# Optimization experiments

Measured on AMD Instinct MI355X. Metric: run time of the kernel, lower is better.

Reference implementation:

```python
import jax, jax.numpy as jnp
import numpy as np

B, N, FEAT, BB, LD = 512, 50, 300, 300, 2048
D1 = BB + FEAT        # 600 = s_with_bb dim
D2 = 2 * D1           # 1200 = combined dim


def _fc(x, w, b):
    # ReLUWithWeightNormFC: weight-norm is a reparametrization of a plain
    # linear, so math-equivalently ReLU(x @ W^T + b).
    return jax.nn.relu(x @ w.T + b)


def setup_inputs() -> dict:
    key = jax.random.key(0)
    ks = jax.random.split(key, 32)

    def p(k, shape):
        return jax.random.normal(k, shape, dtype=jnp.float32) * 0.02

    inp = {
        "l": jax.random.normal(ks[0], (B, LD), dtype=jnp.float32),
        "s": jax.random.normal(ks[1], (B, N, FEAT), dtype=jnp.float32),
        "ps": jax.random.uniform(ks[2], (B, N, 4), dtype=jnp.float32),
        "mask_s": jax.random.randint(ks[3], (B,), 0, 50, dtype=jnp.int32),
        "bb_w": p(ks[4], (BB, 10)),       "bb_b": p(ks[5], (BB,)),
        "fa1_w": p(ks[6], (D1, D1)),      "fa1_b": p(ks[7], (D1,)),
        "fa2_w": p(ks[8], (D1, D1)),      "fa2_b": p(ks[9], (D1,)),
        "fa3_w": p(ks[10], (D2, D2)),     "fa3_b": p(ks[11], (D2,)),
        "fa4_w": p(ks[12], (D2, D2)),     "fa4_b": p(ks[13], (D2,)),
        "fa5_w": p(ks[14], (D2, D2)),     "fa5_b": p(ks[15], (D2,)),
        "lp1_w": p(ks[16], (D2, LD)),     "lp1_b": p(ks[17], (D2,)),
        "lp2_w": p(ks[18], (D2, LD)),     "lp2_b": p(ks[19], (D2,)),
        "out_w": p(ks[20], (FEAT, D2)),   "out_b": p(ks[21], (FEAT,)),
    }
    return inp


def reference(l, s, ps, mask_s,
              bb_w, bb_b, fa1_w, fa1_b, fa2_w, fa2_b, fa3_w, fa3_b,
              fa4_w, fa4_b, fa5_w, fa5_b, lp1_w, lp1_b, lp2_w, lp2_b,
              out_w, out_b):
    # ---- bb_process ----
    size = ps[..., 2:] - ps[..., :2]                       # [B,N,2]
    centre = ps[..., :2] + 0.5 * size                      # [B,N,2]
    area = (size[..., 0] * size[..., 1])[..., None]        # [B,N,1]
    shape = (size[..., 0] / (size[..., 1] + 1e-14))[..., None]
    bb_in = jnp.concatenate([ps, size, centre, area, shape], axis=-1)  # [B,N,10]
    bb = _fc(bb_in, bb_w, bb_b)                            # [B,N,BB]

    s_bb = jnp.concatenate([s, bb], axis=-1)               # [B,N,D1]

    # ---- masked adjacency bias (order of assignments preserved) ----
    i = jnp.arange(N)
    mx = jnp.maximum(i[None, :], i[:, None])               # [N,N]
    m1 = mx[None, :, :] < mask_s[:, None, None]            # [B,N,N]
    m2 = i[None, :, None] >= mask_s[:, None, None]         # row index >= mask_s
    inf_tmp = jnp.where(m1 | m2, 0.0, -jnp.inf)
    inf_tmp = jnp.where(jnp.eye(N, dtype=bool)[None], -jnp.inf, inf_tmp)
    inf_tmp = inf_tmp.at[:, 0, 0].set(
        jnp.where(mask_s == 1, 0.0, inf_tmp[:, 0, 0]))

    # l projections are identical across the 50 nodes -> compute once, broadcast
    lp1 = _fc(l, lp1_w, lp1_b)[:, None, :]                 # [B,1,D2]
    lp2 = _fc(l, lp2_w, lp2_b)[:, None, :]                 # [B,1,D2]

    # ---- one GNN iteration (it=1) ----
    combined = jnp.concatenate(
        [s_bb, _fc(s_bb, fa1_w, fa1_b) * _fc(s_bb, fa2_w, fa2_b)], axis=-1)  # [B,N,D2]
    l_masked_source = _fc(combined, fa3_w, fa3_b) * lp1    # [B,N,D2]
    adj = jnp.einsum('bnd,bmd->bnm', _fc(combined, fa4_w, fa4_b),
                     l_masked_source)                      # [B,N,N]
    adj = jax.nn.softmax(adj + inf_tmp, axis=2)
    prepared = _fc(combined, fa5_w, fa5_b) * lp2           # [B,N,D2]
    messages = _fc(jnp.einsum('bnm,bmd->bnd', adj, prepared), out_w, out_b)
    s_out = jnp.concatenate([s, messages], axis=-1)        # [B,N,2*FEAT]

    output_mask = (i[None, :] < mask_s[:, None])[:, :, None]  # [B,N,1]
    return s_out * output_mask.astype(s_out.dtype), adj
```

## Files before the change

### kernel.cpp

```cpp
#include <hip/hip_runtime.h>
#include <stdint.h>

typedef unsigned short u16;
typedef unsigned int u32;
typedef __attribute__((ext_vector_type(8))) __bf16 bf16x8;
typedef __attribute__((ext_vector_type(4))) float f32x4;

#define DEVINL static __device__ __forceinline__

DEVINL u16 f2bf(float x) {
  u32 u = __float_as_uint(x);
  return (u16)((u + (((u >> 16) & 1u) + 0x7fffu)) >> 16);
}
DEVINL float bf2f(u16 h) { return __uint_as_float(((u32)h) << 16); }

DEVINL void async16(const void* g, void* l) {
  void* g2 = const_cast<void*>(g);
  __builtin_amdgcn_global_load_lds((__attribute__((address_space(1))) void*)g2,
                                   (__attribute__((address_space(3))) void*)l,
                                   16, 0, 0);
}

DEVINL void swz_xy(int& bx, int& by) {
  const int gx = (int)gridDim.x;
// ... 82 lines not shown
  const int p1 = ((c1 & 3) ^ ((c1 >> 3) & 3)) * 8;
  const long ao0 = (long)(c0 >> 2) * lda + p0;
  const long ao1 = (long)(c1 >> 2) * lda + p1;
  const long bo0 = (long)(c0 >> 2) * ldw + p0;
  const long bo1 = (long)(c1 >> 2) * ldw + p1;

  int aoffs[4], boffs[4];
#pragma unroll
  for (int k = 0; k < 4; ++k) {
    const int ra = wr + mrow + 16 * k;
    const int rb = wc + mrow + 16 * k;
    aoffs[k] = ra * 32 + ((q ^ ((ra >> 1) & 3)) << 3);
    boffs[k] = rb * 32 + ((q ^ ((rb >> 1) & 3)) << 3);
  }

  auto issueF = [&](int ph) {
    const long ta = (long)(ph >> 1) * 32;
    const u16* sa = (ph & 1) ? Alp : Ahp;
    const u16* sb = (ph & 1) ? Blp : Bhp;
    u16* d = S + (ph & 3) * 8192;
    async16(sa + ta + ao0, d + c0 * 8);
    async16(sa + ta + ao1, d + c1 * 8);
    async16(sb + ta + bo0, d + 4096 + c0 * 8);
    async16(sb + ta + bo1, d + 4096 + c1 * 8);
  };

  const int total = 2 * ksteps;
  issueF(0); issueF(1); if (total > 2) issueF(2);
  bf16x8 ah[4], bh[4];
  for (int i = 0; i < ksteps; ++i) {
    {
      const int rem = total - 1 - 2 * i;
      if (rem >= 2)      asm volatile("s_waitcnt vmcnt(8)" ::: "memory");
      else               asm volatile("s_waitcnt vmcnt(4)" ::: "memory");
      __builtin_amdgcn_sched_barrier(0);
      __builtin_amdgcn_s_barrier();
      __builtin_amdgcn_sched_barrier(0);
      if (2 * i + 3 < total) issueF(2 * i + 3);
      const u16* hb = S + ((2 * i) & 3) * 8192;
#pragma unroll
      for (int k = 0; k < 4; ++k) {
        ah[k] = *(const bf16x8*)(hb + aoffs[k]);
        bh[k] = *(const bf16x8*)(hb + 4096 + boffs[k]);
      }
#pragma unroll
      for (int mi = 0; mi < 4; ++mi)
#pragma unroll
        for (int nj = 0; nj < 4; ++nj)
          acc[mi][nj] = __builtin_amdgcn_mfma_f32_16x16x32_bf16(
              ah[mi], bh[nj], acc[mi][nj], 0, 0, 0);
    }
    {
      const int rem = total - 2 - 2 * i;
      if (rem >= 2)      asm volatile("s_waitcnt vmcnt(8)" ::: "memory");
      else if (rem == 1) asm volatile("s_waitcnt vmcnt(4)" ::: "memory");
      else               asm volatile("s_waitcnt vmcnt(0)" ::: "memory");
      __builtin_amdgcn_sched_barrier(0);
      __builtin_amdgcn_s_barrier();
      __builtin_amdgcn_sched_barrier(0);
      if (2 * i + 4 < total) issueF(2 * i + 4);
      const u16* hb = S + ((2 * i + 1) & 3) * 8192;
      bf16x8 al[4], bl[4];
#pragma unroll
      for (int k = 0; k < 4; ++k) {
        al[k] = *(const bf16x8*)(hb + aoffs[k]);
        bl[k] = *(const bf16x8*)(hb + 4096 + boffs[k]);
      }
#pragma unroll
      for (int mi = 0; mi < 4; ++mi)
#pragma unroll
        for (int nj = 0; nj < 4; ++nj)
          acc[mi][nj] = __builtin_amdgcn_mfma_f32_16x16x32_bf16(
              al[mi], bh[nj], acc[mi][nj], 0, 0, 0);
#pragma unroll
      for (int mi = 0; mi < 4; ++mi)
#pragma unroll
        for (int nj = 0; nj < 4; ++nj)
          acc[mi][nj] = __builtin_amdgcn_mfma_f32_16x16x32_bf16(
              ah[mi], bl[nj], acc[mi][nj], 0, 0, 0);
    }
  }
}

DEVINL void gemm_core1(const u16* Ab, const u16* Bb, int lda, int ldw,
                       int ksteps, u16* As, u16* Bs, f32x4 (&acc)[4][4]) {
  const int tid = threadIdx.x;
  const int lane = tid & 63;
  const int wv = tid >> 6;
  const int wr = (wv >> 1) * 64;
  const int wc = (wv & 1) * 64;
  const int mrow = lane & 15;
  const int q = lane >> 4;

  const int c0 = tid, c1 = tid + 256;
  const int p0 = ((c0 & 3) ^ ((c0 >> 3) & 3)) * 8;
  const int p1 = ((c1 & 3) ^ ((c1 >> 3) & 3)) * 8;
  const long ao0 = (long)(c0 >> 2) * lda + p0;
  const long ao1 = (long)(c1 >> 2) * lda + p1;
  const long bo0 = (long)(c0 >> 2) * ldw + p0;
  const long bo1 = (long)(c1 >> 2) * ldw + p1;

  int aoffs[4], boffs[4];
#pragma unroll
  for (int k = 0; k < 4; ++k) {
    const int ra = wr + mrow + 16 * k;
    const int rb = wc + mrow + 16 * k;
    aoffs[k] = ra * 32 + ((q ^ ((ra >> 1) & 3)) << 3);
    boffs[k] = rb * 32 + ((q ^ ((rb >> 1) & 3)) << 3);
  }

  auto issue = [&](int sl, int t) {
    const long ta = (long)t * 32;
    u16* dA = As + sl * 4096;
    u16* dB = Bs + sl * 4096;
    async16(Ab + ta + ao0, dA + c0 * 8);
    async16(Ab + ta + ao1, dA + c1 * 8);
    async16(Bb + ta + bo0, dB + c0 * 8);
    async16(Bb + ta + bo1, dB + c1 * 8);
  };

  const int npro = ksteps < 3 ? ksteps : 3;
  for (int j = 0; j < npro; ++j) issue(j, j);
  int cs = 0, is = 3;
  for (int i = 0; i < ksteps; ++i) {
    const int rem = ksteps - 1 - i;
    if (rem >= 2)      asm volatile("s_waitcnt vmcnt(8)" ::: "memory");
    else if (rem == 1) asm volatile("s_waitcnt vmcnt(4)" ::: "memory");
    else               asm volatile("s_waitcnt vmcnt(0)" ::: "memory");
    __builtin_amdgcn_sched_barrier(0);
    __builtin_amdgcn_s_barrier();
    __builtin_amdgcn_sched_barrier(0);
    if (i + 3 < ksteps) { issue(is, i + 3); is = (is + 1) & 3; }
    const u16* Sa = As + cs * 4096;
    const u16* Sb = Bs + cs * 4096;
    cs = (cs + 1) & 3;
    bf16x8 af[4], bv[4];
#pragma unroll
    for (int k = 0; k < 4; ++k) af[k] = *(const bf16x8*)(Sa + aoffs[k]);
#pragma unroll
    for (int k = 0; k < 4; ++k) bv[k] = *(const bf16x8*)(Sb + boffs[k]);
#pragma unroll
    for (int mi = 0; mi < 4; ++mi)
#pragma unroll
      for (int nj = 0; nj < 4; ++nj)
        acc[mi][nj] = __builtin_amdgcn_mfma_f32_16x16x32_bf16(
            af[mi], bv[nj], acc[mi][nj], 0, 0, 0);
  }
}

DEVINL void gemm_core2(const u16* const Aph[3], const u16* const B1ph[3],
                       const u16* const B2ph[3], int lda, int ldw, int ksteps,
                       u16* As, u16* B1s, u16* B2s, f32x4 (&a1)[4][4],
                       f32x4 (&a2)[4][4]) {
  const int tid = threadIdx.x;
  const int lane = tid & 63;
  const int wv = tid >> 6;
  const int wr = (wv >> 1) * 64;
  const int wc = (wv & 1) * 64;
  const int mrow = lane & 15;
  const int q = lane >> 4;

  const int c0 = tid, c1 = tid + 256;
  const int p0 = ((c0 & 3) ^ ((c0 >> 3) & 3)) * 8;
  const int p1 = ((c1 & 3) ^ ((c1 >> 3) & 3)) * 8;
  const long ao0 = (long)(c0 >> 2) * lda + p0;
  const long ao1 = (long)(c1 >> 2) * lda + p1;
  const long bo0 = (long)(c0 >> 2) * ldw + p0;
  const long bo1 = (long)(c1 >> 2) * ldw + p1;

  int aoffs[4], boffs[4];
#pragma unroll
  for (int k = 0; k < 4; ++k) {
    const int ra = wr + mrow + 16 * k;
    const int rb = wc + mrow + 16 * k;
    aoffs[k] = ra * 32 + ((q ^ ((ra >> 1) & 3)) << 3);
    boffs[k] = rb * 32 + ((q ^ ((rb >> 1) & 3)) << 3);
  }

  const u16* Aa1 = Aph[1]; const u16* Ba1 = B1ph[1]; const u16* Ca1 = B2ph[1];
  const u16* Aa2 = Aph[2]; const u16* Ba2 = B1ph[2]; const u16* Ca2 = B2ph[2];
  const u16* An = Aph[0];  const u16* Bn = B1ph[0];  const u16* Cn = B2ph[0];
  int tn = 0, pn = 0;
  const int total = 3 * ksteps;

  auto issue = [&](int sl) {
    const u16* ga = An + (long)tn * 32;
    const u16* g1 = Bn + (long)tn * 32;
    const u16* g2 = Cn + (long)tn * 32;
    u16* dA = As + sl * 4096;
    u16* d1 = B1s + sl * 4096;
    u16* d2 = B2s + sl * 4096;
    async16(ga + ao0, dA + c0 * 8);
    async16(ga + ao1, dA + c1 * 8);
    async16(g1 + bo0, d1 + c0 * 8);
    async16(g1 + bo1, d1 + c1 * 8);
    async16(g2 + bo0, d2 + c0 * 8);
    async16(g2 + bo1, d2 + c1 * 8);
    if (++tn == ksteps) {
      tn = 0; ++pn;
      if (pn == 1) { An = Aa1; Bn = Ba1; Cn = Ca1; }
      else if (pn == 2) { An = Aa2; Bn = Ba2; Cn = Ca2; }
    }
  };

  issue(0);
  issue(1);
  int slot = 0;
  for (int i = 0; i < total; ++i) {
    if (i + 1 < total) asm volatile("s_waitcnt vmcnt(6)" ::: "memory");
    else               asm volatile("s_waitcnt vmcnt(0)" ::: "memory");
    __builtin_amdgcn_sched_barrier(0);
    __builtin_amdgcn_s_barrier();
    __builtin_amdgcn_sched_barrier(0);
    if (i + 2 < total) {
      int s2 = slot + 2; if (s2 >= 3) s2 -= 3;
      issue(s2);
    }
    const u16* Sa = As + slot * 4096;
    const u16* S1 = B1s + slot * 4096;
    const u16* S2 = B2s + slot * 4096;
    bf16x8 af[4], b1v[4], b2v[4];
#pragma unroll
    for (int k = 0; k < 4; ++k) af[k] = *(const bf16x8*)(Sa + aoffs[k]);
#pragma unroll
    for (int k = 0; k < 4; ++k) b1v[k] = *(const bf16x8*)(S1 + boffs[k]);
#pragma unroll
    for (int k = 0; k < 4; ++k) b2v[k] = *(const bf16x8*)(S2 + boffs[k]);
#pragma unroll
    for (int mi = 0; mi < 4; ++mi)
#pragma unroll
      for (int nj = 0; nj < 4; ++nj)
        a1[mi][nj] = __builtin_amdgcn_mfma_f32_16x16x32_bf16(
            af[mi], b1v[nj], a1[mi][nj], 0, 0, 0);
#pragma unroll
    for (int mi = 0; mi < 4; ++mi)
#pragma unroll
      for (int nj = 0; nj < 4; ++nj)
        a2[mi][nj] = __builtin_amdgcn_mfma_f32_16x16x32_bf16(
            af[mi], b2v[nj], a2[mi][nj], 0, 0, 0);
    if (++slot == 3) slot = 0;
  }
}

#define GEMM_EPI_IDX                                                    \
  const int lane = threadIdx.x & 63, wv = threadIdx.x >> 6;             \
  const int wr = (wv >> 1) * 64, wc = (wv & 1) * 64;                    \
  const int mcol = lane & 15, q = lane >> 4;                            \
  const int gm0 = by * 128, gn0 = bx * 128;

__global__ __launch_bounds__(256) void k_gemm_fa12(const u16* Ah, const u16* Al,
    const u16* W1h, const u16* W1l, const u16* W2h, const u16* W2l,
    const float* bias, u16* Chi, u16* Clo) {
  __shared__ __align__(16) u16 As[12288], B1s[12288], B2s[12288];
  int bx, by; swz_xy(bx, by);
  const size_t arow = (size_t)by * 128 * 1280;
  const size_t wrow = (size_t)bx * 128 * 640;
  const u16* Aph[3]  = {Ah + arow, Al + arow, Ah + arow};
  const u16* B1ph[3] = {W1h + wrow, W1h + wrow, W1l + wrow};
  const u16* B2ph[3] = {W2h + wrow, W2h + wrow, W2l + wrow};
  f32x4 a1[4][4] = {}, a2[4][4] = {};
  gemm_core2(Aph, B1ph, B2ph, 1280, 640, 20, As, B1s, B2s, a1, a2);
  GEMM_EPI_IDX
#pragma unroll
  for (int mi = 0; mi < 4; ++mi)
#pragma unroll
    for (int r = 0; r < 4; ++r) {
      int grow = gm0 + wr + mi * 16 + q * 4 + r;
#pragma unroll
      for (int ni = 0; ni < 4; ++ni) {
        int gcol = gn0 + wc + ni * 16 + mcol;
        float v1 = fmaxf(a1[mi][ni][r] + bias[gcol], 0.f);
        float v2 = fmaxf(a2[mi][ni][r] + bias[640 + gcol], 0.f);
        float y = v1 * v2;
        u16 h = f2bf(y);
        Chi[(size_t)grow * 1280 + 640 + gcol] = h;
        Clo[(size_t)grow * 1280 + 640 + gcol] = f2bf(y - bf2f(h));
      }
    }
}

__global__ __launch_bounds__(256) void k_gemm_lp(const u16* Ah, const u16* Al,
    const u16* Wh, const u16* Wl, const float* bias, float* outp) {
  __shared__ __align__(16) u16 S[32768];
  int bx, by; swz_xy(bx, by);
  const size_t arow = (size_t)by * 128 * 2048;
  const size_t wrow = (size_t)bx * 128 * 2048;
  f32x4 acc[4][4] = {};
  gemm_fused3(Ah + arow, Al + arow, Wh + wrow, Wl + wrow, 2048, 2048, 64, S,
              acc);
  GEMM_EPI_IDX
#pragma unroll
  for (int mi = 0; mi < 4; ++mi)
#pragma unroll
    for (int r = 0; r < 4; ++r) {
      int grow = gm0 + wr + mi * 16 + q * 4 + r;
#pragma unroll
      for (int ni = 0; ni < 4; ++ni) {
        int gcol = gn0 + wc + ni * 16 + mcol;
        outp[(size_t)grow * 2560 + gcol] = fmaxf(acc[mi][ni][r] + bias[gcol], 0.f);
      }
    }
}

__global__ __launch_bounds__(512, 2) void k_gemm_fa34(const u16* Ah,
    const u16* Al, const u16* Wh, const u16* Wl, const float* b34,
    const float* lp_o, u16* fa3h, u16* fa3l, u16* fa4h, u16* fa4l, int r0) {
  __shared__ __align__(16) u16 S[2][4][8192];
  int bx, by; swz_xy(bx, by);
  const int tid = threadIdx.x;
  const int lane = tid & 63, wv = tid >> 6;
  const int wm = wv >> 2, wn = wv & 3;
  const int mrow = lane & 15, q = lane >> 4;

  const size_t arow = (size_t)by * 256 * 1280;
  const size_t wrow = (size_t)bx * 256 * 1280;
  const u16* mats[4] = {Ah + arow, Al + arow, Wh + wrow, Wl + wrow};

  long soff[2];
#pragma unroll
  for (int j = 0; j < 2; ++j) {
    const int c = j * 512 + tid;
    soff[j] = (long)(c >> 2) * 1280 + ((c & 3) ^ ((c >> 3) & 3)) * 8;
  }
  int aoffs[8], boffs[4];
#pragma unroll
  for (int k = 0; k < 8; ++k) {
    const int r = wm * 128 + k * 16 + mrow;
    aoffs[k] = r * 32 + ((q ^ ((r >> 1) & 3)) << 3);
  }
#pragma unroll
  for (int k = 0; k < 4; ++k) {
    const int r = wn * 64 + k * 16 + mrow;
    boffs[k] = r * 32 + ((q ^ ((r >> 1) & 3)) << 3);
  }

  f32x4 acc[8][4] = {};
  const int ks = 40;

#pragma unroll
  for (int m = 0; m < 4; ++m) {
    async16(mats[m] + soff[0], &S[0][m][tid * 8]);
    async16(mats[m] + soff[1], &S[0][m][(512 + tid) * 8]);
  }
  asm volatile("s_waitcnt vmcnt(0)" ::: "memory");
  __builtin_amdgcn_sched_barrier(0);
  __builtin_amdgcn_s_barrier();

  for (int t = 0; t < ks; ++t) {
    const int cur = t & 1;
    const long ta = (long)(t + 1) * 32;
    const bool more = (t + 1 < ks);
    bf16x8 bh[4], bl[4];
#pragma unroll
    for (int p = 0; p < 8; ++p) {
      if (p == 0) {
#pragma unroll
        for (int k = 0; k < 4; ++k) {
          bh[k] = *(const bf16x8*)(&S[cur][2][0] + boffs[k]);
          bl[k] = *(const bf16x8*)(&S[cur][3][0] + boffs[k]);
        }
      }
      bf16x8 ah = *(const bf16x8*)(&S[cur][0][0] + aoffs[p]);
      bf16x8 al = *(const bf16x8*)(&S[cur][1][0] + aoffs[p]);
      if (p < 4 && more) {
        async16(mats[p] + ta + soff[0], &S[cur ^ 1][p][tid * 8]);
        async16(mats[p] + ta + soff[1], &S[cur ^ 1][p][(512 + tid) * 8]);
      }
      __builtin_amdgcn_s_barrier();
      asm volatile("s_waitcnt lgkmcnt(0)" ::: "memory");
      __builtin_amdgcn_sched_barrier(0);
      __builtin_amdgcn_s_setprio(1);
#pragma unroll
      for (int j = 0; j < 4; ++j)
        acc[p][j] = __builtin_amdgcn_mfma_f32_16x16x32_bf16(ah, bh[j],
                                                            acc[p][j], 0, 0, 0);
#pragma unroll
      for (int j = 0; j < 4; ++j)
        acc[p][j] = __builtin_amdgcn_mfma_f32_16x16x32_bf16(al, bh[j],
                                                            acc[p][j], 0, 0, 0);
#pragma unroll
      for (int j = 0; j < 4; ++j)
        acc[p][j] = __builtin_amdgcn_mfma_f32_16x16x32_bf16(ah, bl[j],
                                                            acc[p][j], 0, 0, 0);
      __builtin_amdgcn_s_setprio(0);
      __builtin_amdgcn_s_barrier();
    }
    if (more) {
      asm volatile("s_waitcnt vmcnt(0)" ::: "memory");
      __builtin_amdgcn_sched_barrier(0);
      __builtin_amdgcn_s_barrier();
    }
  }

  const int gm0 = by * 256, gn0 = bx * 256;
  const int seg = (gn0 >= 1280);
  u16* dsth = seg ? fa4h : fa3h;
  u16* dstl = seg ? fa4l : fa3l;
#pragma unroll
  for (int p = 0; p < 8; ++p)
#pragma unroll
    for (int r = 0; r < 4; ++r) {
      const int grow = gm0 + wm * 128 + p * 16 + q * 4 + r;
      const int b = (r0 + grow) / 50;
      const float* lpb = lp_o + (size_t)b * 2560;
#pragma unroll
      for (int j = 0; j < 4; ++j) {
        const int gcol = gn0 + wn * 64 + j * 16 + mrow;
        const int c = gcol - seg * 1280;
        float v = fmaxf(acc[p][j][r] + b34[gcol], 0.f);
        if (!seg) v *= lpb[c];
        if (c < 1216) {
          u16 h = f2bf(v);
          dsth[(size_t)grow * 1216 + c] = h;
          dstl[(size_t)grow * 1216 + c] = f2bf(v - bf2f(h));
        }
      }
    }
}

__global__ __launch_bounds__(256) void k_gemm_fa5(const u16* Ah,
    const u16* W5h, const float* b5, const float* lp_o, u16* fa5o, int r0) {
  __shared__ __align__(16) u16 S[32768];
  int bx, by; swz_xy(bx, by);
  const size_t arow = (size_t)by * 128 * 1280;
  const size_t wrow = (size_t)bx * 128 * 1280;
  f32x4 acc[4][4] = {};
  gemm_core1(Ah + arow, W5h + wrow, 1280, 1280, 40, S, S + 16384, acc);
  GEMM_EPI_IDX
#pragma unroll
  for (int mi = 0; mi < 4; ++mi)
#pragma unroll
    for (int r = 0; r < 4; ++r) {
      int grow = gm0 + wr + mi * 16 + q * 4 + r;
      int b = (r0 + grow) / 50;
      const float* lpb = lp_o + (size_t)b * 2560 + 1280;
#pragma unroll
      for (int ni = 0; ni < 4; ++ni) {
        int gcol = gn0 + wc + ni * 16 + mcol;
        float v = fmaxf(acc[mi][ni][r] + b5[gcol], 0.f) * lpb[gcol];
        if (gcol < 1216) fa5o[(size_t)grow * 1216 + gcol] = f2bf(v);
      }
    }
}

__global__ __launch_bounds__(256) void k_gemm_out(const u16* A, const u16* Wh,
    const float* bias, const int* mask_s, float* outp, int r0) {
  __shared__ __align__(16) u16 S[32768];
  int bx, by; swz_xy(bx, by);
  const size_t arow = (size_t)by * 128 * 1216;
  const size_t wrow = (size_t)bx * 128 * 1216;
  f32x4 acc[4][4] = {};
  gemm_core1(A + arow, Wh + wrow, 1216, 1216, 38, S, S + 16384, acc);
  GEMM_EPI_IDX
#pragma unroll
  for (int mi = 0; mi < 4; ++mi)
#pragma unroll
    for (int r = 0; r < 4; ++r) {
      int grow = r0 + gm0 + wr + mi * 16 + q * 4 + r;
      int b = grow / 50;
      int n = grow - b * 50;
      float keep = (n < mask_s[b]) ? 1.f : 0.f;
#pragma unroll
      for (int ni = 0; ni < 4; ++ni) {
        int gcol = gn0 + wc + ni * 16 + mcol;
        float v = fmaxf(acc[mi][ni][r] + bias[gcol], 0.f) * keep;
        if (gcol < 300) outp[(size_t)grow * 600 + 300 + gcol] = v;
      }
    }
}

__global__ __launch_bounds__(256) void k_attn(const u16* fa3h, const u16* fa3l,
    const u16* fa4h, const u16* fa4l, const u16* fa5o, const int* mask_s,
    float* adj_out, u16* msg, int b0) {
  __shared__ __align__(16) u16 stg[32768];
  __shared__ float Ssc[64 * 64];
  const int bl = blockIdx.x;
  const int bg = b0 + bl;
  const int tid = threadIdx.x, lane = tid & 63, wv = tid >> 6;
  const int mrow = lane & 15, q = lane >> 4;
  const size_t base = (size_t)bl * 50 * 1216;

  {
    const int srow = tid >> 2;
    const int srcRow = srow < 50 ? srow : 49;
    const size_t gsoff = base + (size_t)srcRow * 1216 +
                         (size_t)(((tid & 3) ^ ((tid >> 3) & 3)) * 8);
    auto issueP1 = [&](int sl, int s) {
      const int p = (s >= 76) ? 2 : (s >= 38 ? 1 : 0);
      const int t = s - p * 38;
      const u16* Ap = (p == 1) ? fa4l : fa4h;
      const u16* Bp = (p == 2) ? fa3l : fa3h;
      u16* d = stg + sl * 4096;
      async16(Ap + gsoff + (size_t)t * 32, d + tid * 8);
      async16(Bp + gsoff + (size_t)t * 32, d + 2048 + tid * 8);
    };
    const int ra = wv * 16 + mrow;
    const int aoff = ra * 32 + ((q ^ ((ra >> 1) & 3)) << 3);
    int boff[4];
#pragma unroll
    for (int ni = 0; ni < 4; ++ni) {
      const int rb = ni * 16 + mrow;
      boff[ni] = rb * 32 + ((q ^ ((rb >> 1) & 3)) << 3);
    }
    for (int j = 0; j < 7; ++j) issueP1(j, j);
    f32x4 acc[4] = {};
    int cs = 0, is = 7;
    for (int i = 0; i < 114; ++i) {
      const int rem = 113 - i;
      if (rem >= 6)      asm volatile("s_waitcnt vmcnt(12)" ::: "memory");
      else if (rem == 5) asm volatile("s_waitcnt vmcnt(10)" ::: "memory");
      else if (rem == 4) asm volatile("s_waitcnt vmcnt(8)" ::: "memory");
      else if (rem == 3) asm volatile("s_waitcnt vmcnt(6)" ::: "memory");
      else if (rem == 2) asm volatile("s_waitcnt vmcnt(4)" ::: "memory");
      else if (rem == 1) asm volatile("s_waitcnt vmcnt(2)" ::: "memory");
      else               asm volatile("s_waitcnt vmcnt(0)" ::: "memory");
      __builtin_amdgcn_sched_barrier(0);
      __builtin_amdgcn_s_barrier();
      __builtin_amdgcn_sched_barrier(0);
      if (i + 7 < 114) { issueP1(is, i + 7); if (++is == 8) is = 0; }
      const u16* d = stg + cs * 4096;
      if (++cs == 8) cs = 0;
      bf16x8 af = *(const bf16x8*)(d + aoff);
#pragma unroll
      for (int ni = 0; ni < 4; ++ni) {
        bf16x8 bv = *(const bf16x8*)(d + 2048 + boff[ni]);
        acc[ni] =
            __builtin_amdgcn_mfma_f32_16x16x32_bf16(af, bv, acc[ni], 0, 0, 0);
      }
    }
#pragma unroll
    for (int ni = 0; ni < 4; ++ni)
#pragma unroll
      for (int r = 0; r < 4; ++r)
        Ssc[(wv * 16 + q * 4 + r) * 64 + ni * 16 + mrow] = acc[ni][r];
  }
  __syncthreads();

  const int c0 = tid, c1 = tid + 256;
  const int m0 = c0 >> 3, d0 = (c0 & 7) * 8;
  const int m1 = c1 >> 3, d1 = (c1 & 7) * 8;
  const size_t g0 = base + (size_t)(m0 < 50 ? m0 : 49) * 1216 + d0;
  const size_t g1 = base + (size_t)(m1 < 50 ? m1 : 49) * 1216 + d1;
  auto issueP3 = [&](int sl, int s) {
    u16* d = stg + sl * 4096;
    async16(fa5o + g0 + (size_t)s * 64, d + c0 * 8);
    async16(fa5o + g1 + (size_t)s * 64, d + c1 * 8);
  };
  for (int j = 0; j < 7; ++j) issueP3(j, j);

  {
    const int mk = mask_s[bg];
    for (int n = wv; n < 50; n += 4) {
      int mm = lane;
      float v = -__builtin_inff();
      if (mm < 50) {
        int mx2 = n > mm ? n : mm;
        bool valid = (mx2 < mk) || (n >= mk);
        if (mm == n) valid = false;
        if (n == 0 && mm == 0 && mk == 1) valid = true;
        if (valid) v = Ssc[n * 64 + mm];
      }
      float mx = v;
      for (int o = 32; o > 0; o >>= 1) mx = fmaxf(mx, __shfl_down(mx, o));
      mx = __shfl(mx, 0);
      float e = __expf(v - mx);
      float sm = e;
      for (int o = 32; o > 0; o >>= 1) sm += __shfl_down(sm, o);
      sm = __shfl(sm, 0);
      float pv = e / sm;
      if (mm < 50) {
        adj_out[((size_t)bg * 50 + n) * 50 + mm] = pv;
        Ssc[n * 64 + mm] = pv;
      } else {
        Ssc[n * 64 + mm] = 0.f;
      }
    }
  }
  __syncthreads();

  {
    int cs = 0, is = 7;
    for (int dt = 0; dt < 19; ++dt) {
      const int rem = 18 - dt;
      if (rem >= 6)      asm volatile("s_waitcnt vmcnt(12)" ::: "memory");
      else if (rem == 5) asm volatile("s_waitcnt vmcnt(10)" ::: "memory");
      else if (rem == 4) asm volatile("s_waitcnt vmcnt(8)" ::: "memory");
      else if (rem == 3) asm volatile("s_waitcnt vmcnt(6)" ::: "memory");
      else if (rem == 2) asm volatile("s_waitcnt vmcnt(4)" ::: "memory");
      else if (rem == 1) asm volatile("s_waitcnt vmcnt(2)" ::: "memory");
      else               asm volatile("s_waitcnt vmcnt(0)" ::: "memory");
      __builtin_amdgcn_sched_barrier(0);
      __builtin_amdgcn_s_barrier();
      __builtin_amdgcn_sched_barrier(0);
      if (dt + 7 < 19) { issueP3(is, dt + 7); if (++is == 8) is = 0; }
      const u16* d = stg + cs * 4096;
      if (++cs == 8) cs = 0;
      f32x4 a3[4] = {};
#pragma unroll
      for (int ks = 0; ks < 2; ++ks) {
        bf16x8 af;
#pragma unroll
        for (int j = 0; j < 8; ++j)
          af[j] = (__bf16)Ssc[(wv * 16 + mrow) * 64 + ks * 32 + q * 8 + j];
#pragma unroll
        for (int ni = 0; ni < 4; ++ni) {
          bf16x8 bv;
#pragma unroll
          for (int j = 0; j < 8; ++j)
            bv[j] = *(const __bf16*)(d + (ks * 32 + q * 8 + j) * 64 + ni * 16 + mrow);
          a3[ni] = __builtin_amdgcn_mfma_f32_16x16x32_bf16(af, bv, a3[ni], 0, 0, 0);
        }
      }
#pragma unroll
      for (int ni = 0; ni < 4; ++ni)
#pragma unroll
        for (int r = 0; r < 4; ++r) {
          int n = wv * 16 + q * 4 + r;
          if (n < 50)
            msg[((size_t)bl * 50 + n) * 1216 + dt * 64 + ni * 16 + mrow] =
                f2bf(a3[ni][r]);
        }
    }
  }
}

extern "C" void kernel_launch(void* const* d_in, const int* in_sizes, int n_in,
                              void* d_out_, int out_size, void* d_ws,
                              size_t ws_size, hipStream_t stream) {
  (void)in_sizes; (void)n_in; (void)out_size;
  const float* l_in = (const float*)d_in[0];
  const float* s_in = (const float*)d_in[1];
  const float* ps   = (const float*)d_in[2];
  const int*   msk  = (const int*)d_in[3];
  const float* bbw  = (const float*)d_in[4];
  const float* bbb  = (const float*)d_in[5];
  const float* fa1w = (const float*)d_in[6];
  const float* fa1b = (const float*)d_in[7];
  const float* fa2w = (const float*)d_in[8];
  const float* fa2b = (const float*)d_in[9];
  const float* fa3w = (const float*)d_in[10];
  const float* fa3b = (const float*)d_in[11];
  const float* fa4w = (const float*)d_in[12];
  const float* fa4b = (const float*)d_in[13];
  const float* fa5w = (const float*)d_in[14];
  const float* fa5b = (const float*)d_in[15];
  const float* lp1w = (const float*)d_in[16];
  const float* lp1b = (const float*)d_in[17];
  const float* lp2w = (const float*)d_in[18];
  const float* lp2b = (const float*)d_in[19];
  const float* outw = (const float*)d_in[20];
  const float* outb = (const float*)d_in[21];
  float* outp = (float*)d_out_;

  char* wsb = (char*)d_ws;
  size_t off = 0;
  auto alloc = [&](size_t bytes) -> char* {
    char* p = wsb + off;
    off = (off + bytes + 255) & ~(size_t)255;
    return p;
  };
  u16*   l_hi   = (u16*)alloc(512ull * 2048 * 2);
  u16*   l_lo   = (u16*)alloc(512ull * 2048 * 2);
  u16*   Wout   = (u16*)alloc(384ull * 1216 * 2);
  float* b_fa12 = (float*)alloc(1280 * 4);
  float* b_fa34 = (float*)alloc(2560 * 4);
  float* b_fa5  = (float*)alloc(1280 * 4);
  float* b_lp   = (float*)alloc(2560 * 4);
  float* b_out  = (float*)alloc(384 * 4);
  float* lp_o   = (float*)alloc(512ull * 2560 * 4);
  u16*   slab   = (u16*)alloc(10485760ull * 2);
  u16* Wlph   = slab;
  u16* Wlpl   = slab + 5242880;
  u16* Wfa1h  = slab;
  u16* Wfa1l  = slab + 409600;
  u16* Wfa2h  = slab + 819200;
  u16* Wfa2l  = slab + 1228800;
  u16* Wfa34h = slab + 1638400;
  u16* Wfa34l = slab + 4915200;
  u16* Wfa5h  = slab + 8192000;

  size_t ws_eff = ws_size ? ws_size : (size_t)512 * 1024 * 1024;
  long RN = 6400;
  const long opts[3] = {25600, 12800, 6400};
  for (int i = 0; i < 3; ++i) {
    size_t need = off + (size_t)17280 * opts[i] + 8 * 256;
    if (need <= ws_eff) { RN = opts[i]; break; }
  }
  u16*  Chi  = (u16*)alloc((size_t)RN * 1280 * 2);
  u16*  Clo  = (u16*)alloc((size_t)RN * 1280 * 2);
  u16*  fa5o = (u16*)alloc((size_t)RN * 1216 * 2);
  u16*  fa3h = (u16*)alloc((size_t)RN * 1216 * 2);
  u16*  fa3l = (u16*)alloc((size_t)RN * 1216 * 2);
  u16*  fa4h = (u16*)alloc((size_t)RN * 1216 * 2);
  u16*  fa4l = (u16*)alloc((size_t)RN * 1216 * 2);
  u16*  msg  = Chi;
  float* adj_o = outp + 15360000;

  dim3 T(256);
  k_pack_bias<<<dim3(3), T, 0, stream>>>(fa1b, 600, b_fa12, 640);
  k_pack_bias<<<dim3(3), T, 0, stream>>>(fa2b, 600, b_fa12 + 640, 640);
  k_pack_bias<<<dim3(5), T, 0, stream>>>(fa3b, 1200, b_fa34, 1280);
  k_pack_bias<<<dim3(5), T, 0, stream>>>(fa4b, 1200, b_fa34 + 1280, 1280);
  k_pack_bias<<<dim3(5), T, 0, stream>>>(fa5b, 1200, b_fa5, 1280);
  k_pack_bias<<<dim3(5), T, 0, stream>>>(lp1b, 1200, b_lp, 1280);
  k_pack_bias<<<dim3(5), T, 0, stream>>>(lp2b, 1200, b_lp + 1280, 1280);
  k_pack_bias<<<dim3(2), T, 0, stream>>>(outb, 300, b_out, 384);

  auto packw = [&](const float* src, int n, int k, u16* hi, u16* lo, int KP,
                   long total, int gap) {
    k_pack_w<<<dim3((unsigned)((total + 255) / 256)), T, 0, stream>>>(
        src, n, k, hi, lo, KP, total, gap);
  };
  packw(l_in, 512, 2048, l_hi, l_lo, 2048, 512L * 2048, 0);
  packw(outw, 300, 1200, Wout, nullptr, 1216, 384L * 1216, 0);

  packw(lp1w, 1200, 2048, Wlph, Wlpl, 2048, 1280L * 2048, 0);
  packw(lp2w, 1200, 2048, Wlph + 1280 * 2048, Wlpl + 1280 * 2048, 2048,
        1280L * 2048, 0);
  k_gemm_lp<<<dim3(20, 4), T, 0, stream>>>(l_hi, l_lo, Wlph, Wlpl, b_lp, lp_o);

  packw(fa1w, 600, 600, Wfa1h, Wfa1l, 640, 640L * 640, 0);
  packw(fa2w, 600, 600, Wfa2h, Wfa2l, 640, 640L * 640, 0);
  packw(fa3w, 1200, 1200, Wfa34h, Wfa34l, 1280, 1280L * 1280, 1);
  packw(fa4w, 1200, 1200, Wfa34h + 1638400, Wfa34l + 1638400, 1280,
        1280L * 1280, 1);
  packw(fa5w, 1200, 1200, Wfa5h, nullptr, 1280, 1280L * 1280, 1);

  const int nch = (int)(25600 / RN);
  const unsigned gy = (unsigned)(RN / 128);
  for (int c = 0; c < nch; ++c) {
    const int r0 = (int)(c * RN);
    const int b0 = r0 / 50;
    k_bb<<<dim3((unsigned)RN), T, 0, stream>>>(s_in + (size_t)r0 * 300,
                                               ps + (size_t)r0 * 4, bbw, bbb,
                                               msk, Chi, Clo, outp, r0);
    k_gemm_fa12<<<dim3(5, gy), T, 0, stream>>>(Chi, Clo, Wfa1h, Wfa1l, Wfa2h,
                                               Wfa2l, b_fa12, Chi, Clo);
    k_gemm_fa34<<<dim3(10, (unsigned)(RN / 256)), dim3(512), 0, stream>>>(
        Chi, Clo, Wfa34h, Wfa34l, b_fa34, lp_o, fa3h, fa3l, fa4h, fa4l, r0);
    k_gemm_fa5<<<dim3(10, gy), T, 0, stream>>>(Chi, Wfa5h, b_fa5, lp_o, fa5o,
                                               r0);
    k_attn<<<dim3((unsigned)(RN / 50)), T, 0, stream>>>(fa3h, fa3l, fa4h, fa4l,
                                                        fa5o, msk, adj_o, msg,
                                                        b0);
    k_gemm_out<<<dim3(3, gy), T, 0, stream>>>(msg, Wout, b_out, msk, outp, r0);
  }
}
```

Baseline: 1.401 ms.

## Merge fa5 GEMM into fa3/fa4 GEMM launch with 256x256 tiles

Combines the fa3/fa4 split-bf16 GEMM and the single-precision fa5 GEMM into one kernel launch. Blocks with bx>=10 take a new fa5 path that uses 256x256 tiles and 512 threads instead of the old 128x128 gemm_core1. The fa3/fa4 inner loop now handles two A sub-tiles per barrier phase, halving barriers per k-step and regrouping prefetch staging. This removes one launch and tail, improves load balance across CUs, and raises data reuse for fa5, at the cost of a larger heterogeneous kernel whose two block types have different work per block.

```diff
diff --git a/kernel.cpp b/kernel.cpp
--- a/kernel.cpp
+++ b/kernel.cpp
@@ -408,19 +408,18 @@
     }
 }
 
-__global__ __launch_bounds__(512, 2) void k_gemm_fa34(const u16* Ah,
-    const u16* Al, const u16* Wh, const u16* Wl, const float* b34,
-    const float* lp_o, u16* fa3h, u16* fa3l, u16* fa4h, u16* fa4l, int r0) {
+__global__ __launch_bounds__(512, 2) void k_gemm_fa345b(const u16* Ah,
+    const u16* Al, const u16* Wh, const u16* Wl, const u16* W5h,
+    const float* b34, const float* b5, const float* lp_o, u16* fa3h,
+    u16* fa3l, u16* fa4h, u16* fa4l, u16* fa5o, int r0) {
   __shared__ __align__(16) u16 S[2][4][8192];
   int bx, by; swz_xy(bx, by);
   const int tid = threadIdx.x;
   const int lane = tid & 63, wv = tid >> 6;
   const int wm = wv >> 2, wn = wv & 3;
   const int mrow = lane & 15, q = lane >> 4;
-
   const size_t arow = (size_t)by * 256 * 1280;
-  const size_t wrow = (size_t)bx * 256 * 1280;
-  const u16* mats[4] = {Ah + arow, Al + arow, Wh + wrow, Wl + wrow};
+  const int gm0 = by * 256;
 
   long soff[2];
 #pragma unroll
@@ -443,110 +442,166 @@
   f32x4 acc[8][4] = {};
   const int ks = 40;
 
-#pragma unroll
-  for (int m = 0; m < 4; ++m) {
-    async16(mats[m] + soff[0], &S[0][m][tid * 8]);
-    async16(mats[m] + soff[1], &S[0][m][(512 + tid) * 8]);
-  }
-  asm volatile("s_waitcnt vmcnt(0)" ::: "memory");
-  __builtin_amdgcn_sched_barrier(0);
-  __builtin_amdgcn_s_barrier();
-
-  for (int t = 0; t < ks; ++t) {
-    const int cur = t & 1;
-    const long ta = (long)(t + 1) * 32;
-    const bool more = (t + 1 < ks);
-    bf16x8 bh[4], bl[4];
-#pragma unroll
-    for (int p = 0; p < 8; ++p) {
-      if (p == 0) {
-#pragma unroll
-        for (int k = 0; k < 4; ++k) {
-          bh[k] = *(const bf16x8*)(&S[cur][2][0] + boffs[k]);
-          bl[k] = *(const bf16x8*)(&S[cur][3][0] + boffs[k]);
+  if (bx < 10) {
+    const size_t wrow = (size_t)bx * 256 * 1280;
+    const u16* mats[4] = {Ah + arow, Al + arow, Wh + wrow, Wl + wrow};
+    auto stage = [&](int m, long ta, int buf) {
+      async16(mats[m] + ta + soff[0], &S[buf][m][tid * 8]);
+      async16(mats[m] + ta + soff[1], &S[buf][m][(512 + tid) * 8]);
+    };
+#pragma unroll
+    for (int m = 0; m < 4; ++m) stage(m, 0, 0);
+    asm volatile("s_waitcnt vmcnt(0)" ::: "memory");
+    __builtin_amdgcn_sched_barrier(0);
+    __builtin_amdgcn_s_barrier();
+
+    for (int t = 0; t < ks; ++t) {
+      const int cur = t & 1;
+      const long ta = (long)(t + 1) * 32;
+      const bool more = (t + 1 < ks);
+      bf16x8 bh[4], bl[4];
+#pragma unroll
+      for (int p = 0; p < 4; ++p) {
+        if (p == 0) {
+#pragma unroll
+          for (int k = 0; k < 4; ++k) {
+            bh[k] = *(const bf16x8*)(&S[cur][2][0] + boffs[k]);
+            bl[k] = *(const bf16x8*)(&S[cur][3][0] + boffs[k]);
+          }
         }
-      }
-      bf16x8 ah = *(const bf16x8*)(&S[cur][0][0] + aoffs[p]);
-      bf16x8 al = *(const bf16x8*)(&S[cur][1][0] + aoffs[p]);
-      if (p < 4 && more) {
-        async16(mats[p] + ta + soff[0], &S[cur ^ 1][p][tid * 8]);
-        async16(mats[p] + ta + soff[1], &S[cur ^ 1][p][(512 + tid) * 8]);
-      }
-      __builtin_amdgcn_s_barrier();
-      asm volatile("s_waitcnt lgkmcnt(0)" ::: "memory");
-      __builtin_amdgcn_sched_barrier(0);
-      __builtin_amdgcn_s_setprio(1);
-#pragma unroll
-      for (int j = 0; j < 4; ++j)
-        acc[p][j] = __builtin_amdgcn_mfma_f32_16x16x32_bf16(ah, bh[j],
-                                                            acc[p][j], 0, 0, 0);
-#pragma unroll
-      for (int j = 0; j < 4; ++j)
-        acc[p][j] = __builtin_amdgcn_mfma_f32_16x16x32_bf16(al, bh[j],
-                                                            acc[p][j], 0, 0, 0);
-#pragma unroll
-      for (int j = 0; j < 4; ++j)
-        acc[p][j] = __builtin_amdgcn_mfma_f32_16x16x32_bf16(ah, bl[j],
-                                                            acc[p][j], 0, 0, 0);
-      __builtin_amdgcn_s_setprio(0);
-      __builtin_amdgcn_s_barrier();
-    }
-    if (more) {
-      asm volatile("s_waitcnt vmcnt(0)" ::: "memory");
-      __builtin_amdgcn_sched_barrier(0);
-      __builtin_amdgcn_s_barrier();
-    }
-  }
-
-  const int gm0 = by * 256, gn0 = bx * 256;
-  const int seg = (gn0 >= 1280);
-  u16* dsth = seg ? fa4h : fa3h;
-  u16* dstl = seg ? fa4l : fa3l;
-#pragma unroll
-  for (int p = 0; p < 8; ++p)
-#pragma unroll
-    for (int r = 0; r < 4; ++r) {
-      const int grow = gm0 + wm * 128 + p * 16 + q * 4 + r;
-      const int b = (r0 + grow) / 50;
-      const float* lpb = lp_o + (size_t)b * 2560;
-#pragma unroll
-      for (int j = 0; j < 4; ++j) {
-        const int gcol = gn0 + wn * 64 + j * 16 + mrow;
-        const int c = gcol - seg * 1280;
-        float v = fmaxf(acc[p][j][r] + b34[gcol], 0.f);
-        if (!seg) v *= lpb[c];
-        if (c < 1216) {
-          u16 h = f2bf(v);
-          dsth[(size_t)grow * 1216 + c] = h;
-          dstl[(size_t)grow * 1216 + c] = f2bf(v - bf2f(h));
+        bf16x8 a0h = *(const bf16x8*)(&S[cur][0][0] + aoffs[2 * p]);
+        bf16x8 a1h = *(const bf16x8*)(&S[cur][0][0] + aoffs[2 * p + 1]);
+        bf16x8 a0l = *(const bf16x8*)(&S[cur][1][0] + aoffs[2 * p]);
+        bf16x8 a1l = *(const bf16x8*)(&S[cur][1][0] + aoffs[2 * p + 1]);
+        if (more) {
+          if (p == 0)      { stage(0, ta, cur ^ 1); stage(1, ta, cur ^ 1); }
+          else if (p == 1) stage(2, ta, cur ^ 1);
+          else if (p == 2) stage(3, ta, cur ^ 1);
         }
-      }
-    }
-}
-
-__global__ __launch_bounds__(256) void k_gemm_fa5(const u16* Ah,
-    const u16* W5h, const float* b5, const float* lp_o, u16* fa5o, int r0) {
-  __shared__ __align__(16) u16 S[32768];
-  int bx, by; swz_xy(bx, by);
-  const size_t arow = (size_t)by * 128 * 1280;
-  const size_t wrow = (size_t)bx * 128 * 1280;
-  f32x4 acc[4][4] = {};
-  gemm_core1(Ah + arow, W5h + wrow, 1280, 1280, 40, S, S + 16384, acc);
-  GEMM_EPI_IDX
-#pragma unroll
-  for (int mi = 0; mi < 4; ++mi)
-#pragma unroll
-    for (int r = 0; r < 4; ++r) {
-      int grow = gm0 + wr + mi * 16 + q * 4 + r;
-      int b = (r0 + grow) / 50;
-      const float* lpb = lp_o + (size_t)b * 2560 + 1280;
-#pragma unroll
-      for (int ni = 0; ni < 4; ++ni) {
-        int gcol = gn0 + wc + ni * 16 + mcol;
-        float v = fmaxf(acc[mi][ni][r] + b5[gcol], 0.f) * lpb[gcol];
-        if (gcol < 1216) fa5o[(size_t)grow * 1216 + gcol] = f2bf(v);
-      }
-    }
+        __builtin_amdgcn_s_barrier();
+        asm volatile("s_waitcnt lgkmcnt(0)" ::: "memory");
+        __builtin_amdgcn_sched_barrier(0);
+        __builtin_amdgcn_s_setprio(1);
+#pragma unroll
+        for (int j = 0; j < 4; ++j) {
+          acc[2 * p][j] = __builtin_amdgcn_mfma_f32_16x16x32_bf16(
+              a0h, bh[j], acc[2 * p][j], 0, 0, 0);
+          acc[2 * p + 1][j] = __builtin_amdgcn_mfma_f32_16x16x32_bf16(
+              a1h, bh[j], acc[2 * p + 1][j], 0, 0, 0);
+        }
+#pragma unroll
+        for (int j = 0; j < 4; ++j) {
+          acc[2 * p][j] = __builtin_amdgcn_mfma_f32_16x16x32_bf16(
+              a0l, bh[j], acc[2 * p][j], 0, 0, 0);
+          acc[2 * p + 1][j] = __builtin_amdgcn_mfma_f32_16x16x32_bf16(
+              a1l, bh[j], acc[2 * p + 1][j], 0, 0, 0);
+        }
+#pragma unroll
+        for (int j = 0; j < 4; ++j) {
+          acc[2 * p][j] = __builtin_amdgcn_mfma_f32_16x16x32_bf16(
+              a0h, bl[j], acc[2 * p][j], 0, 0, 0);
+          acc[2 * p + 1][j] = __builtin_amdgcn_mfma_f32_16x16x32_bf16(
+              a1h, bl[j], acc[2 * p + 1][j], 0, 0, 0);
+        }
+        __builtin_amdgcn_s_setprio(0);
+        if (p < 3) __builtin_amdgcn_s_barrier();
+      }
+      if (more) {
+        asm volatile("s_waitcnt vmcnt(0)" ::: "memory");
+        __builtin_amdgcn_sched_barrier(0);
+        __builtin_amdgcn_s_barrier();
+      }
+    }
+
+    const int gn0 = bx * 256;
+    const int seg = (gn0 >= 1280);
+    u16* dsth = seg ? fa4h : fa3h;
+    u16* dstl = seg ? fa4l : fa3l;
+#pragma unroll
+    for (int p = 0; p < 8; ++p)
+#pragma unroll
+      for (int r = 0; r < 4; ++r) {
+        const int grow = gm0 + wm * 128 + p * 16 + q * 4 + r;
+        const int b = (r0 + grow) / 50;
+        const float* lpb = lp_o + (size_t)b * 2560;
+#pragma unroll
+        for (int j = 0; j < 4; ++j) {
+          const int gcol = gn0 + wn * 64 + j * 16 + mrow;
+          const int c = gcol - seg * 1280;
+          float v = fmaxf(acc[p][j][r] + b34[gcol], 0.f);
+          if (!seg) v *= lpb[c];
+          if (c < 1216) {
+            u16 h = f2bf(v);
+            dsth[(size_t)grow * 1216 + c] = h;
+            dstl[(size_t)grow * 1216 + c] = f2bf(v - bf2f(h));
+          }
+        }
+      }
+  } else {
+    const size_t wrow = (size_t)(bx - 10) * 256 * 1280;
+    const u16* mats[2] = {Ah + arow, W5h + wrow};
+    auto stage = [&](int m, long ta, int buf) {
+      async16(mats[m] + ta + soff[0], &S[buf][m][tid * 8]);
+      async16(mats[m] + ta + soff[1], &S[buf][m][(512 + tid) * 8]);
+    };
+    stage(0, 0, 0); stage(1, 0, 0);
+    asm volatile("s_waitcnt vmcnt(0)" ::: "memory");
+    __builtin_amdgcn_sched_barrier(0);
+    __builtin_amdgcn_s_barrier();
+
+    for (int t = 0; t < ks; ++t) {
+      const int cur = t & 1;
+      const long ta = (long)(t + 1) * 32;
+      const bool more = (t + 1 < ks);
+      bf16x8 bv[4];
+#pragma unroll
+      for (int p = 0; p < 2; ++p) {
+        if (p == 0) {
+#pragma unroll
+          for (int k = 0; k < 4; ++k)
+            bv[k] = *(const bf16x8*)(&S[cur][1][0] + boffs[k]);
+        }
+        bf16x8 av[4];
+#pragma unroll
+        for (int i = 0; i < 4; ++i)
+          av[i] = *(const bf16x8*)(&S[cur][0][0] + aoffs[4 * p + i]);
+        if (more && p == 0) { stage(0, ta, cur ^ 1); stage(1, ta, cur ^ 1); }
+        __builtin_amdgcn_s_barrier();
+        asm volatile("s_waitcnt lgkmcnt(0)" ::: "memory");
+        __builtin_amdgcn_sched_barrier(0);
+        __builtin_amdgcn_s_setprio(1);
+#pragma unroll
+        for (int i = 0; i < 4; ++i)
+#pragma unroll
+          for (int j = 0; j < 4; ++j)
+            acc[4 * p + i][j] = __builtin_amdgcn_mfma_f32_16x16x32_bf16(
+                av[i], bv[j], acc[4 * p + i][j], 0, 0, 0);
+        __builtin_amdgcn_s_setprio(0);
+        if (p < 1) __builtin_amdgcn_s_barrier();
+      }
+      if (more) {
+        asm volatile("s_waitcnt vmcnt(0)" ::: "memory");
+        __builtin_amdgcn_sched_barrier(0);
+        __builtin_amdgcn_s_barrier();
+      }
+    }
+
+    const int gn0 = (bx - 10) * 256;
+#pragma unroll
+    for (int p = 0; p < 8; ++p)
+#pragma unroll
+      for (int r = 0; r < 4; ++r) {
+        const int grow = gm0 + wm * 128 + p * 16 + q * 4 + r;
+        const int b = (r0 + grow) / 50;
+        const float* lpb = lp_o + (size_t)b * 2560 + 1280;
+#pragma unroll
+        for (int j = 0; j < 4; ++j) {
+          const int gcol = gn0 + wn * 64 + j * 16 + mrow;
+          float v = fmaxf(acc[p][j][r] + b5[gcol], 0.f) * lpb[gcol];
+          if (gcol < 1216) fa5o[(size_t)grow * 1216 + gcol] = f2bf(v);
+        }
+      }
+  }
 }
 
 __global__ __launch_bounds__(256) void k_gemm_out(const u16* A, const u16* Wh,
@@ -842,10 +897,9 @@
                                                msk, Chi, Clo, outp, r0);
     k_gemm_fa12<<<dim3(5, gy), T, 0, stream>>>(Chi, Clo, Wfa1h, Wfa1l, Wfa2h,
                                                Wfa2l, b_fa12, Chi, Clo);
-    k_gemm_fa34<<<dim3(10, (unsigned)(RN / 256)), dim3(512), 0, stream>>>(
-        Chi, Clo, Wfa34h, Wfa34l, b_fa34, lp_o, fa3h, fa3l, fa4h, fa4l, r0);
-    k_gemm_fa5<<<dim3(10, gy), T, 0, stream>>>(Chi, Wfa5h, b_fa5, lp_o, fa5o,
-                                               r0);
+    k_gemm_fa345b<<<dim3(15, (unsigned)(RN / 256)), dim3(512), 0, stream>>>(
+        Chi, Clo, Wfa34h, Wfa34l, Wfa5h, b_fa34, b_fa5, lp_o, fa3h, fa3l,
+        fa4h, fa4l, fa5o, r0);
     k_attn<<<dim3((unsigned)(RN / 50)), T, 0, stream>>>(fa3h, fa3l, fa4h, fa4l,
                                                         fa5o, msk, adj_o, msg,
                                                         b0);
```

After: 1.455 ms. 3.8% more time.

## Use 512 threads in attention kernel, splitting tile columns across wave pairs

Applied to the files above, without the earlier changes.

Doubles the attention kernel's block to 8 waves. Each pair of waves shares a 16-row tile and splits its four column subtiles two apiece, and the async global-to-LDS copies are split so each thread issues one load per stage instead of two, with the vmcnt waits adjusted to match. The aim is more latency hiding and more MFMA issue parallelism per block. In exchange the A fragment is loaded redundantly by both waves of a pair, and LDS use per block limits how many blocks fit per CU.

```diff
diff --git a/kernel.cpp b/kernel.cpp
--- a/kernel.cpp
+++ b/kernel.cpp
@@ -575,7 +575,7 @@
     }
 }
 
-__global__ __launch_bounds__(256) void k_attn(const u16* fa3h, const u16* fa3l,
+__global__ __launch_bounds__(512) void k_attn(const u16* fa3h, const u16* fa3l,
     const u16* fa4h, const u16* fa4l, const u16* fa5o, const int* mask_s,
     float* adj_out, u16* msg, int b0) {
   __shared__ __align__(16) u16 stg[32768];
@@ -583,42 +583,46 @@
   const int bl = blockIdx.x;
   const int bg = b0 + bl;
   const int tid = threadIdx.x, lane = tid & 63, wv = tid >> 6;
+  const int rt = wv >> 1;
+  const int cp = wv & 1;
   const int mrow = lane & 15, q = lane >> 4;
   const size_t base = (size_t)bl * 50 * 1216;
 
   {
-    const int srow = tid >> 2;
+    const int idx = tid & 255;
+    const int half = tid >> 8;
+    const int srow = idx >> 2;
     const int srcRow = srow < 50 ? srow : 49;
     const size_t gsoff = base + (size_t)srcRow * 1216 +
-                         (size_t)(((tid & 3) ^ ((tid >> 3) & 3)) * 8);
+                         (size_t)(((idx & 3) ^ ((idx >> 3) & 3)) * 8);
     auto issueP1 = [&](int sl, int s) {
       const int p = (s >= 76) ? 2 : (s >= 38 ? 1 : 0);
       const int t = s - p * 38;
-      const u16* Ap = (p == 1) ? fa4l : fa4h;
-      const u16* Bp = (p == 2) ? fa3l : fa3h;
-      u16* d = stg + sl * 4096;
-      async16(Ap + gsoff + (size_t)t * 32, d + tid * 8);
-      async16(Bp + gsoff + (size_t)t * 32, d + 2048 + tid * 8);
+      const u16* src;
+      if (half == 0) src = (p == 1) ? fa4l : fa4h;
+      else           src = (p == 2) ? fa3l : fa3h;
+      async16(src + gsoff + (size_t)t * 32,
+              stg + sl * 4096 + half * 2048 + idx * 8);
     };
-    const int ra = wv * 16 + mrow;
+    const int ra = rt * 16 + mrow;
     const int aoff = ra * 32 + ((q ^ ((ra >> 1) & 3)) << 3);
-    int boff[4];
-#pragma unroll
-    for (int ni = 0; ni < 4; ++ni) {
-      const int rb = ni * 16 + mrow;
-      boff[ni] = rb * 32 + ((q ^ ((rb >> 1) & 3)) << 3);
+    int boff[2];
+#pragma unroll
+    for (int j = 0; j < 2; ++j) {
+      const int rb = (2 * cp + j) * 16 + mrow;
+      boff[j] = rb * 32 + ((q ^ ((rb >> 1) & 3)) << 3);
     }
     for (int j = 0; j < 7; ++j) issueP1(j, j);
-    f32x4 acc[4] = {};
+    f32x4 acc[2] = {};
     int cs = 0, is = 7;
     for (int i = 0; i < 114; ++i) {
       const int rem = 113 - i;
-      if (rem >= 6)      asm volatile("s_waitcnt vmcnt(12)" ::: "memory");
-      else if (rem == 5) asm volatile("s_waitcnt vmcnt(10)" ::: "memory");
-      else if (rem == 4) asm volatile("s_waitcnt vmcnt(8)" ::: "memory");
-      else if (rem == 3) asm volatile("s_waitcnt vmcnt(6)" ::: "memory");
-      else if (rem == 2) asm volatile("s_waitcnt vmcnt(4)" ::: "memory");
-      else if (rem == 1) asm volatile("s_waitcnt vmcnt(2)" ::: "memory");
+      if (rem >= 6)      asm volatile("s_waitcnt vmcnt(6)" ::: "memory");
+      else if (rem == 5) asm volatile("s_waitcnt vmcnt(5)" ::: "memory");
+      else if (rem == 4) asm volatile("s_waitcnt vmcnt(4)" ::: "memory");
+      else if (rem == 3) asm volatile("s_waitcnt vmcnt(3)" ::: "memory");
+      else if (rem == 2) asm volatile("s_waitcnt vmcnt(2)" ::: "memory");
+      else if (rem == 1) asm volatile("s_waitcnt vmcnt(1)" ::: "memory");
       else               asm volatile("s_waitcnt vmcnt(0)" ::: "memory");
       __builtin_amdgcn_sched_barrier(0);
       __builtin_amdgcn_s_barrier();
@@ -628,35 +632,30 @@
       if (++cs == 8) cs = 0;
       bf16x8 af = *(const bf16x8*)(d + aoff);
 #pragma unroll
-      for (int ni = 0; ni < 4; ++ni) {
-        bf16x8 bv = *(const bf16x8*)(d + 2048 + boff[ni]);
-        acc[ni] =
-            __builtin_amdgcn_mfma_f32_16x16x32_bf16(af, bv, acc[ni], 0, 0, 0);
-      }
-    }
-#pragma unroll
-    for (int ni = 0; ni < 4; ++ni)
+      for (int j = 0; j < 2; ++j) {
+        bf16x8 bv = *(const bf16x8*)(d + 2048 + boff[j]);
+        acc[j] =
+            __builtin_amdgcn_mfma_f32_16x16x32_bf16(af, bv, acc[j], 0, 0, 0);
+      }
+    }
+#pragma unroll
+    for (int j = 0; j < 2; ++j)
 #pragma unroll
       for (int r = 0; r < 4; ++r)
-        Ssc[(wv * 16 + q * 4 + r) * 64 + ni * 16 + mrow] = acc[ni][r];
+        Ssc[(rt * 16 + q * 4 + r) * 64 + (2 * cp + j) * 16 + mrow] = acc[j][r];
   }
   __syncthreads();
 
-  const int c0 = tid, c1 = tid + 256;
-  const int m0 = c0 >> 3, d0 = (c0 & 7) * 8;
-  const int m1 = c1 >> 3, d1 = (c1 & 7) * 8;
+  const int m0 = tid >> 3, d0 = (tid & 7) * 8;
   const size_t g0 = base + (size_t)(m0 < 50 ? m0 : 49) * 1216 + d0;
-  const size_t g1 = base + (size_t)(m1 < 50 ? m1 : 49) * 1216 + d1;
   auto issueP3 = [&](int sl, int s) {
-    u16* d = stg + sl * 4096;
-    async16(fa5o + g0 + (size_t)s * 64, d + c0 * 8);
-    async16(fa5o + g1 + (size_t)s * 64, d + c1 * 8);
+    async16(fa5o + g0 + (size_t)s * 64, stg + sl * 4096 + tid * 8);
   };
   for (int j = 0; j < 7; ++j) issueP3(j, j);
 
   {
     const int mk = mask_s[bg];
-    for (int n = wv; n < 50; n += 4) {
+    for (int n = wv; n < 50; n += 8) {
       int mm = lane;
       float v = -__builtin_inff();
       if (mm < 50) {
@@ -688,12 +687,12 @@
     int cs = 0, is = 7;
     for (int dt = 0; dt < 19; ++dt) {
       const int rem = 18 - dt;
-      if (rem >= 6)      asm volatile("s_waitcnt vmcnt(12)" ::: "memory");
-      else if (rem == 5) asm volatile("s_waitcnt vmcnt(10)" ::: "memory");
-      else if (rem == 4) asm volatile("s_waitcnt vmcnt(8)" ::: "memory");
-      else if (rem == 3) asm volatile("s_waitcnt vmcnt(6)" ::: "memory");
-      else if (rem == 2) asm volatile("s_waitcnt vmcnt(4)" ::: "memory");
-      else if (rem == 1) asm volatile("s_waitcnt vmcnt(2)" ::: "memory");
+      if (rem >= 6)      asm volatile("s_waitcnt vmcnt(6)" ::: "memory");
+      else if (rem == 5) asm volatile("s_waitcnt vmcnt(5)" ::: "memory");
+      else if (rem == 4) asm volatile("s_waitcnt vmcnt(4)" ::: "memory");
+      else if (rem == 3) asm volatile("s_waitcnt vmcnt(3)" ::: "memory");
+      else if (rem == 2) asm volatile("s_waitcnt vmcnt(2)" ::: "memory");
+      else if (rem == 1) asm volatile("s_waitcnt vmcnt(1)" ::: "memory");
       else               asm volatile("s_waitcnt vmcnt(0)" ::: "memory");
       __builtin_amdgcn_sched_barrier(0);
       __builtin_amdgcn_s_barrier();
@@ -701,30 +700,31 @@
       if (dt + 7 < 19) { issueP3(is, dt + 7); if (++is == 8) is = 0; }
       const u16* d = stg + cs * 4096;
       if (++cs == 8) cs = 0;
-      f32x4 a3[4] = {};
+      f32x4 a3[2] = {};
 #pragma unroll
       for (int ks = 0; ks < 2; ++ks) {
         bf16x8 af;
 #pragma unroll
         for (int j = 0; j < 8; ++j)
-          af[j] = (__bf16)Ssc[(wv * 16 + mrow) * 64 + ks * 32 + q * 8 + j];
-#pragma unroll
-        for (int ni = 0; ni < 4; ++ni) {
+          af[j] = (__bf16)Ssc[(rt * 16 + mrow) * 64 + ks * 32 + q * 8 + j];
+#pragma unroll
+        for (int jj = 0; jj < 2; ++jj) {
+          const int ni = 2 * cp + jj;
           bf16x8 bv;
 #pragma unroll
           for (int j = 0; j < 8; ++j)
             bv[j] = *(const __bf16*)(d + (ks * 32 + q * 8 + j) * 64 + ni * 16 + mrow);
-          a3[ni] = __builtin_amdgcn_mfma_f32_16x16x32_bf16(af, bv, a3[ni], 0, 0, 0);
+          a3[jj] = __builtin_amdgcn_mfma_f32_16x16x32_bf16(af, bv, a3[jj], 0, 0, 0);
         }
       }
 #pragma unroll
-      for (int ni = 0; ni < 4; ++ni)
+      for (int jj = 0; jj < 2; ++jj)
 #pragma unroll
         for (int r = 0; r < 4; ++r) {
-          int n = wv * 16 + q * 4 + r;
+          int n = rt * 16 + q * 4 + r;
           if (n < 50)
-            msg[((size_t)bl * 50 + n) * 1216 + dt * 64 + ni * 16 + mrow] =
-                f2bf(a3[ni][r]);
+            msg[((size_t)bl * 50 + n) * 1216 + dt * 64 + (2 * cp + jj) * 16 + mrow] =
+                f2bf(a3[jj][r]);
         }
     }
   }
@@ -846,9 +846,8 @@
         Chi, Clo, Wfa34h, Wfa34l, b_fa34, lp_o, fa3h, fa3l, fa4h, fa4l, r0);
     k_gemm_fa5<<<dim3(10, gy), T, 0, stream>>>(Chi, Wfa5h, b_fa5, lp_o, fa5o,
                                                r0);
-    k_attn<<<dim3((unsigned)(RN / 50)), T, 0, stream>>>(fa3h, fa3l, fa4h, fa4l,
-                                                        fa5o, msk, adj_o, msg,
-                                                        b0);
+    k_attn<<<dim3((unsigned)(RN / 50)), dim3(512), 0, stream>>>(
+        fa3h, fa3l, fa4h, fa4l, fa5o, msk, adj_o, msg, b0);
     k_gemm_out<<<dim3(3, gy), T, 0, stream>>>(msg, Wout, b_out, msk, outp, r0);
   }
 }
```

New measurement: 1.520 ms. +8.4%, slower.
